# Performance work log

Hardware: AMD Instinct MI355X
Metric: run time of the kernel (lower is better)

## Reference

```python
import jax, jax.numpy as jnp
import numpy as np

M, K, N = 2048, 4096, 11008
Q_ABS_MAX = 128.0  # x_scaled_abs_max_fp for w8a8
Q_MIN, Q_MAX = -128, 127


def setup_inputs() -> dict:
    key = jax.random.key(0)
    k1, k2, k3, k4 = jax.random.split(key, 4)
    x = jax.random.normal(k1, (M, K), dtype=jnp.float32)
    # pre-quantized int8 weight, stored [K, N] (transposed layout as in quantize_weights)
    w_q = jax.random.randint(k2, (K, N), Q_MIN, Q_MAX + 1, dtype=jnp.int32).astype(jnp.int8)
    bias = jax.random.normal(k3, (N,), dtype=jnp.float32) * 0.01
    # per-tensor weight dequant scale (q_scale of the quantized weight)
    y_scale = jax.random.uniform(k4, (1,), dtype=jnp.float32, minval=0.001, maxval=0.02)
    return {"x": x, "w_q": w_q, "bias": bias, "y_scale": y_scale}


def reference(x, w_q, bias, y_scale):
    # dynamic per-tensor activation quantization: scale = max|x| / 128
    x_scale = jnp.max(jnp.abs(x)) / jnp.float32(Q_ABS_MAX)
    x_q = jnp.clip(jnp.round(x / x_scale), Q_MIN, Q_MAX).astype(jnp.int8)
    c = jnp.matmul(x_q.astype(jnp.int32), w_q.astype(jnp.int32))
    # dequantize + bias
    y = c.astype(jnp.float32) * (x_scale * y_scale[0]) + bias
    return y
```

## Files before the change

### kernel.cpp

```cpp
#include <hip/hip_runtime.h>
#include <stdint.h>

#define M_DIM 2048
#define K_DIM 4096
#define N_DIM 11008

typedef int v4i __attribute__((ext_vector_type(4)));

#define WS_XQ_OFF   65536ull
#define WS_WT_OFF   8454144ull
#define WS_FULL_BYTES (8454144ull + 45088768ull)
#define WS_SMALL_BYTES 8454144ull

static __device__ __forceinline__ void llds16(const void* g, void* l) {
  __builtin_amdgcn_global_load_lds(
      reinterpret_cast<const uint32_t __attribute__((address_space(1)))*>(
          reinterpret_cast<uintptr_t>(g)),
      reinterpret_cast<uint32_t __attribute__((address_space(3)))*>(
          reinterpret_cast<uintptr_t>(l)),
      16, 0, 0);
}

__global__ __launch_bounds__(256) void absmax_kernel(const float* __restrict__ x,
                                                     float* __restrict__ part) {
  __shared__ float red[256];
  const int g = blockIdx.x * 256 + threadIdx.x;
  const float4* x4 = reinterpret_cast<const float4*>(x);
  float m = 0.f;
#pragma unroll
  for (int i = 0; i < 8; ++i) {
    float4 v = x4[(size_t)i * 262144 + g];
    m = fmaxf(m, fmaxf(fmaxf(fabsf(v.x), fabsf(v.y)),
                       fmaxf(fabsf(v.z), fabsf(v.w))));
  }
  red[threadIdx.x] = m;
  __syncthreads();
  for (int s = 128; s > 0; s >>= 1) {
    if (threadIdx.x < s) red[threadIdx.x] = fmaxf(red[threadIdx.x], red[threadIdx.x + s]);
    __syncthreads();
  }
  if (threadIdx.x == 0) part[blockIdx.x] = red[0];
}

__global__ __launch_bounds__(256) void finalize_scale(const float* __restrict__ part,
                                                      const float* __restrict__ y_scale,
                                                      float* __restrict__ scales) {
  __shared__ float red[256];
  const int t = threadIdx.x;
  float m = fmaxf(fmaxf(part[t], part[t + 256]), fmaxf(part[t + 512], part[t + 768]));
  red[t] = m;
  __syncthreads();
  for (int s = 128; s > 0; s >>= 1) {
    if (t < s) red[t] = fmaxf(red[t], red[t + s]);
    __syncthreads();
  }
  if (t == 0) {
    float xs = red[0] * (1.0f / 128.0f);
    scales[0] = xs;
    scales[1] = xs * y_scale[0];
  }
}

__global__ __launch_bounds__(256) void quant_kernel(const float* __restrict__ x,
                                                    const float* __restrict__ scales,
                                                    signed char* __restrict__ xq) {
  const float s = scales[0];
  const size_t t = (size_t)blockIdx.x * 256 + threadIdx.x;
  const float4* x4 = reinterpret_cast<const float4*>(x) + t * 4;
  v4i o;
#pragma unroll
  for (int i = 0; i < 4; ++i) {
    float4 v = x4[i];
    int q0 = (int)rintf(v.x / s);
    int q1 = (int)rintf(v.y / s);
    int q2 = (int)rintf(v.z / s);
    int q3 = (int)rintf(v.w / s);
    q0 = max(-128, min(127, q0));
    q1 = max(-128, min(127, q1));
    q2 = max(-128, min(127, q2));
    q3 = max(-128, min(127, q3));
    o[i] = (q0 & 255) | ((q1 & 255) << 8) | ((q2 & 255) << 16) | ((q3 & 255) << 24);
  }
  *reinterpret_cast<v4i*>(xq + t * 16) = o;
}

__global__ __launch_bounds__(256) void transpose_pack(const int* __restrict__ w,
                                                      signed char* __restrict__ wt) {
  __shared__ int tile[64 * 65];
  const int t = threadIdx.x;
  const int n0 = blockIdx.x * 64;
  const int k0 = blockIdx.y * 64;
#pragma unroll
  for (int p = 0; p < 4; ++p) {
    const int id = p * 256 + t;
    const int r = id >> 4;
    const int c4 = id & 15;
    v4i v = *reinterpret_cast<const v4i*>(w + (size_t)(k0 + r) * N_DIM + n0 + c4 * 4);
    tile[r * 65 + c4 * 4 + 0] = v[0];
    tile[r * 65 + c4 * 4 + 1] = v[1];
    tile[r * 65 + c4 * 4 + 2] = v[2];
    tile[r * 65 + c4 * 4 + 3] = v[3];
  }
  __syncthreads();
  const int nl = t >> 2;
  const int kseg = t & 3;
  v4i o;
#pragma unroll
  for (int q = 0; q < 4; ++q) {
    const int kb = kseg * 16 + q * 4;
    int b0 = tile[(kb + 0) * 65 + nl] & 255;
    int b1 = tile[(kb + 1) * 65 + nl] & 255;
    int b2 = tile[(kb + 2) * 65 + nl] & 255;
    int b3 = tile[(kb + 3) * 65 + nl] & 255;
    o[q] = b0 | (b1 << 8) | (b2 << 16) | (b3 << 24);
  }
  *reinterpret_cast<v4i*>(wt + (size_t)(n0 + nl) * K_DIM + k0 + kseg * 16) = o;
}

__global__ __launch_bounds__(256) void gemm_i8(
    const signed char* __restrict__ xq, const signed char* __restrict__ wt,
    const float* __restrict__ scales, const float* __restrict__ bias,
    float* __restrict__ y) {
  __shared__ __align__(16) signed char lds_a[128 * 64];
  __shared__ __align__(16) signed char lds_b[128 * 64];
  const int tid = threadIdx.x;
  const int m0 = blockIdx.y * 128;
  const int n0 = blockIdx.x * 128;

  const int srow = tid >> 2;
  const int sseg = tid & 3;
  const int sgseg = sseg ^ ((srow ^ (srow >> 2)) & 3);
  const signed char* ga0 = xq + (size_t)(m0 + srow) * K_DIM + sgseg * 16;
  const signed char* gb0 = wt + (size_t)(n0 + srow) * K_DIM + sgseg * 16;
  signed char* la0 = lds_a + tid * 16;
  signed char* lb0 = lds_b + tid * 16;

  const int lane = tid & 63;
  const int wid = tid >> 6;
  const int wr = wid >> 1;
  const int wc = wid & 1;
  const int l15 = lane & 15;
  const int kc = lane >> 4;
  const int rslot = (kc ^ ((l15 ^ (l15 >> 2)) & 3)) * 16;
  const signed char* pa = lds_a + (wr * 64 + l15) * 64 + rslot;
  const signed char* pb = lds_b + (wc * 64 + l15) * 64 + rslot;

  v4i acc[4][4] = {};

  for (int kt = 0; kt < K_DIM / 64; ++kt) {
    const int ko = kt * 64;
    llds16(ga0 + ko, la0);
    llds16(ga0 + ko + (size_t)64 * K_DIM, la0 + 4096);
    llds16(gb0 + ko, lb0);
    llds16(gb0 + ko + (size_t)64 * K_DIM, lb0 + 4096);
    __syncthreads();
    v4i a4[4], b4[4];
#pragma unroll
    for (int m = 0; m < 4; ++m) a4[m] = *reinterpret_cast<const v4i*>(pa + m * 1024);
#pragma unroll
    for (int n = 0; n < 4; ++n) b4[n] = *reinterpret_cast<const v4i*>(pb + n * 1024);
#pragma unroll
    for (int m = 0; m < 4; ++m)
#pragma unroll
      for (int n = 0; n < 4; ++n)
        acc[m][n] = __builtin_amdgcn_mfma_i32_16x16x64_i8(a4[m], b4[n], acc[m][n], 0, 0, 0);
    __syncthreads();
  }

  const float s = scales[1];
#pragma unroll
  for (int n = 0; n < 4; ++n) {
    const int col = n0 + wc * 64 + n * 16 + l15;
    const float bv = bias[col];
#pragma unroll
    for (int m = 0; m < 4; ++m) {
      const int r0 = m0 + wr * 64 + m * 16 + kc * 4;
#pragma unroll
      for (int j = 0; j < 4; ++j)
        y[(size_t)(r0 + j) * N_DIM + col] = (float)acc[m][n][j] * s + bv;
    }
  }
}

#if defined(__has_builtin)
#if __has_builtin(__builtin_amdgcn_sdot4)
#define HAVE_SDOT4 1
#endif
#endif

static __device__ __forceinline__ int dot4(int a, int b, int c) {
#ifdef HAVE_SDOT4
  return __builtin_amdgcn_sdot4(a, b, c, false);
#else
  c += (int)(signed char)(a) * (int)(signed char)(b);
  c += (int)(signed char)(a >> 8) * (int)(signed char)(b >> 8);
  c += (int)(signed char)(a >> 16) * (int)(signed char)(b >> 16);
  c += (int)(signed char)(a >> 24) * (int)(signed char)(b >> 24);
  return c;
#endif
}

__global__ __launch_bounds__(256) void gemm_fallback(
    const signed char* __restrict__ xq, const int* __restrict__ w,
    const float* __restrict__ scales, const float* __restrict__ bias,
    float* __restrict__ y) {
  __shared__ int lds_a[64 * 17];
  __shared__ int lds_b[64 * 17];
  const int t = threadIdx.x;
  const int m0 = blockIdx.y * 64;
  const int n0 = blockIdx.x * 64;
  const int my = (t >> 4) * 4;
  const int nx = (t & 15) * 4;
  int acc[4][4] = {};
  for (int kt = 0; kt < K_DIM / 64; ++kt) {
    const int k0 = kt * 64;
    {
      const int r = t >> 2, sg = t & 3;
      v4i v = *reinterpret_cast<const v4i*>(xq + (size_t)(m0 + r) * K_DIM + k0 + sg * 16);
      lds_a[r * 17 + sg * 4 + 0] = v[0];
      lds_a[r * 17 + sg * 4 + 1] = v[1];
      lds_a[r * 17 + sg * 4 + 2] = v[2];
      lds_a[r * 17 + sg * 4 + 3] = v[3];
    }
    {
      const int n = t & 63, bkk = (t >> 6) * 4;
#pragma unroll
      for (int q = 0; q < 4; ++q) {
        const int kk = bkk + q;
        int b0 = w[(size_t)(k0 + kk * 4 + 0) * N_DIM + n0 + n] & 255;
        int b1 = w[(size_t)(k0 + kk * 4 + 1) * N_DIM + n0 + n] & 255;
        int b2 = w[(size_t)(k0 + kk * 4 + 2) * N_DIM + n0 + n] & 255;
        int b3 = w[(size_t)(k0 + kk * 4 + 3) * N_DIM + n0 + n] & 255;
        lds_b[n * 17 + kk] = b0 | (b1 << 8) | (b2 << 16) | (b3 << 24);
      }
    }
    __syncthreads();
#pragma unroll
    for (int kk = 0; kk < 16; ++kk) {
      int a[4], b[4];
#pragma unroll
      for (int i = 0; i < 4; ++i) a[i] = lds_a[(my + i) * 17 + kk];
#pragma unroll
      for (int j = 0; j < 4; ++j) b[j] = lds_b[(nx + j) * 17 + kk];
#pragma unroll
      for (int i = 0; i < 4; ++i)
#pragma unroll
        for (int j = 0; j < 4; ++j) acc[i][j] = dot4(a[i], b[j], acc[i][j]);
    }
    __syncthreads();
  }
  const float s = scales[1];
#pragma unroll
  for (int i = 0; i < 4; ++i)
#pragma unroll
    for (int j = 0; j < 4; ++j)
      y[(size_t)(m0 + my + i) * N_DIM + n0 + nx + j] =
          (float)acc[i][j] * s + bias[n0 + nx + j];
}

extern "C" void kernel_launch(void* const* d_in, const int* in_sizes, int n_in,
                              void* d_out, int out_size, void* d_ws, size_t ws_size,
                              hipStream_t stream) {
  (void)in_sizes; (void)n_in; (void)out_size;
  const float* x = (const float*)d_in[0];
  const int* w = (const int*)d_in[1];
  const float* bias = (const float*)d_in[2];
  const float* yscale = (const float*)d_in[3];
  float* y = (float*)d_out;
  char* ws = (char*)d_ws;
  float* scales = (float*)(ws);
  float* part = (float*)(ws + 1024);
  signed char* xq = (signed char*)(ws + WS_XQ_OFF);
  signed char* wt = (signed char*)(ws + WS_WT_OFF);

  if (ws_size < WS_SMALL_BYTES) return;

  absmax_kernel<<<1024, 256, 0, stream>>>(x, part);
  finalize_scale<<<1, 256, 0, stream>>>(part, yscale, scales);
  quant_kernel<<<2048, 256, 0, stream>>>(x, scales, xq);
  if (ws_size >= WS_FULL_BYTES) {
    transpose_pack<<<dim3(N_DIM / 64, K_DIM / 64), 256, 0, stream>>>(w, wt);
    gemm_i8<<<dim3(N_DIM / 128, M_DIM / 128), 256, 0, stream>>>(xq, wt, scales, bias, y);
  } else {
    gemm_fallback<<<dim3(N_DIM / 64, M_DIM / 64), 256, 0, stream>>>(xq, w, scales, bias, y);
  }
}
```

Baseline: 191.7 us.

## Triple-buffer int8 GEMM with 128x256 tiles and swizzled block order

Replaces the single-buffered 128x128 int8 MFMA GEMM with a 128x256 tile kernel that uses a three-stage LDS ring. Global-to-LDS loads for tile k+2 are issued before computing tile k, with a single barrier per iteration. A 1D grid with an XCD-aware swizzle maps blocks to tiles for better L2 reuse. The aim is to hide load latency and raise MFMA density per LDS read. In exchange, register pressure rises to 32 accumulators per wave, and LDS use grows to 72KB per block, which may limit occupancy.

```diff
diff --git a/kernel.cpp b/kernel.cpp
--- a/kernel.cpp
+++ b/kernel.cpp
@@ -117,64 +117,104 @@
   *reinterpret_cast<v4i*>(wt + (size_t)(n0 + nl) * K_DIM + k0 + kseg * 16) = o;
 }
 
-__global__ __launch_bounds__(256) void gemm_i8(
+#define TILE_B 24576
+#define NT_K   (K_DIM / 64)
+
+__global__ __launch_bounds__(256, 2) void gemm_i8_v2(
     const signed char* __restrict__ xq, const signed char* __restrict__ wt,
     const float* __restrict__ scales, const float* __restrict__ bias,
     float* __restrict__ y) {
-  __shared__ __align__(16) signed char lds_a[128 * 64];
-  __shared__ __align__(16) signed char lds_b[128 * 64];
+  __shared__ __align__(16) signed char smem[3 * TILE_B];
   const int tid = threadIdx.x;
-  const int m0 = blockIdx.y * 128;
-  const int n0 = blockIdx.x * 128;
+
+  const int bid = blockIdx.x;
+  const int swz = (bid & 7) * 86 + (bid >> 3);
+  const int m0 = (swz & 15) * 128;
+  const int n0 = (swz >> 4) * 256;
 
   const int srow = tid >> 2;
   const int sseg = tid & 3;
   const int sgseg = sseg ^ ((srow ^ (srow >> 2)) & 3);
-  const signed char* ga0 = xq + (size_t)(m0 + srow) * K_DIM + sgseg * 16;
-  const signed char* gb0 = wt + (size_t)(n0 + srow) * K_DIM + sgseg * 16;
-  signed char* la0 = lds_a + tid * 16;
-  signed char* lb0 = lds_b + tid * 16;
+  const signed char* gA = xq + (size_t)(m0 + srow) * K_DIM + sgseg * 16;
+  const signed char* gB = wt + (size_t)(n0 + srow) * K_DIM + sgseg * 16;
+  signed char* const l0 = smem + tid * 16;
+
+#define STAGE(kt, soff)                                                   \
+  do {                                                                    \
+    const size_t ko_ = (size_t)(kt) * 64;                                 \
+    llds16(gA + ko_,                       l0 + (soff));                  \
+    llds16(gA + ko_ + (size_t)64 * K_DIM,  l0 + (soff) + 4096);           \
+    llds16(gB + ko_,                       l0 + (soff) + 8192);           \
+    llds16(gB + ko_ + (size_t)64 * K_DIM,  l0 + (soff) + 12288);          \
+    llds16(gB + ko_ + (size_t)128 * K_DIM, l0 + (soff) + 16384);          \
+    llds16(gB + ko_ + (size_t)192 * K_DIM, l0 + (soff) + 20480);          \
+  } while (0)
 
   const int lane = tid & 63;
   const int wid = tid >> 6;
-  const int wr = wid >> 1;
-  const int wc = wid & 1;
+  const int wm = wid >> 1;
+  const int wn = wid & 1;
   const int l15 = lane & 15;
   const int kc = lane >> 4;
   const int rslot = (kc ^ ((l15 ^ (l15 >> 2)) & 3)) * 16;
-  const signed char* pa = lds_a + (wr * 64 + l15) * 64 + rslot;
-  const signed char* pb = lds_b + (wc * 64 + l15) * 64 + rslot;
-
-  v4i acc[4][4] = {};
-
-  for (int kt = 0; kt < K_DIM / 64; ++kt) {
-    const int ko = kt * 64;
-    llds16(ga0 + ko, la0);
-    llds16(ga0 + ko + (size_t)64 * K_DIM, la0 + 4096);
-    llds16(gb0 + ko, lb0);
-    llds16(gb0 + ko + (size_t)64 * K_DIM, lb0 + 4096);
-    __syncthreads();
-    v4i a4[4], b4[4];
-#pragma unroll
-    for (int m = 0; m < 4; ++m) a4[m] = *reinterpret_cast<const v4i*>(pa + m * 1024);
-#pragma unroll
-    for (int n = 0; n < 4; ++n) b4[n] = *reinterpret_cast<const v4i*>(pb + n * 1024);
-#pragma unroll
-    for (int m = 0; m < 4; ++m)
-#pragma unroll
-      for (int n = 0; n < 4; ++n)
-        acc[m][n] = __builtin_amdgcn_mfma_i32_16x16x64_i8(a4[m], b4[n], acc[m][n], 0, 0, 0);
-    __syncthreads();
-  }
+  const int cA = (wm * 64 + l15) * 64 + rslot;
+  const int cB = 8192 + (wn * 128 + l15) * 64 + rslot;
+
+  v4i acc[4][8] = {};
+
+#define COMPUTE(roff)                                                        \
+  do {                                                                       \
+    const signed char* bp_ = smem + (roff);                                  \
+    v4i a_[4], b_[8];                                                        \
+    _Pragma("unroll")                                                        \
+    for (int m_ = 0; m_ < 4; ++m_)                                           \
+      a_[m_] = *reinterpret_cast<const v4i*>(bp_ + cA + m_ * 1024);          \
+    _Pragma("unroll")                                                        \
+    for (int n_ = 0; n_ < 8; ++n_)                                           \
+      b_[n_] = *reinterpret_cast<const v4i*>(bp_ + cB + n_ * 1024);          \
+    _Pragma("unroll")                                                        \
+    for (int m_ = 0; m_ < 4; ++m_)                                           \
+      _Pragma("unroll")                                                      \
+      for (int n_ = 0; n_ < 8; ++n_)                                         \
+        acc[m_][n_] = __builtin_amdgcn_mfma_i32_16x16x64_i8(                 \
+            a_[m_], b_[n_], acc[m_][n_], 0, 0, 0);                           \
+  } while (0)
+
+  STAGE(0, 0);
+  STAGE(1, TILE_B);
+
+  int rOff = 0;
+  int sOff = 2 * TILE_B;
+  for (int t = 0; t < NT_K - 2; ++t) {
+    asm volatile("s_waitcnt vmcnt(6)" ::: "memory");
+    __builtin_amdgcn_s_barrier();
+    __builtin_amdgcn_sched_barrier(0);
+    STAGE(t + 2, sOff);
+    COMPUTE(rOff);
+    rOff = (rOff == 2 * TILE_B) ? 0 : rOff + TILE_B;
+    sOff = (sOff == 2 * TILE_B) ? 0 : sOff + TILE_B;
+  }
+  asm volatile("s_waitcnt vmcnt(6)" ::: "memory");
+  __builtin_amdgcn_s_barrier();
+  __builtin_amdgcn_sched_barrier(0);
+  COMPUTE(rOff);
+  rOff = (rOff == 2 * TILE_B) ? 0 : rOff + TILE_B;
+  asm volatile("s_waitcnt vmcnt(0)" ::: "memory");
+  __builtin_amdgcn_s_barrier();
+  __builtin_amdgcn_sched_barrier(0);
+  COMPUTE(rOff);
+
+#undef STAGE
+#undef COMPUTE
 
   const float s = scales[1];
 #pragma unroll
-  for (int n = 0; n < 4; ++n) {
-    const int col = n0 + wc * 64 + n * 16 + l15;
+  for (int n = 0; n < 8; ++n) {
+    const int col = n0 + wn * 128 + n * 16 + l15;
     const float bv = bias[col];
 #pragma unroll
     for (int m = 0; m < 4; ++m) {
-      const int r0 = m0 + wr * 64 + m * 16 + kc * 4;
+      const int r0 = m0 + wm * 64 + m * 16 + kc * 4;
 #pragma unroll
       for (int j = 0; j < 4; ++j)
         y[(size_t)(r0 + j) * N_DIM + col] = (float)acc[m][n][j] * s + bv;
@@ -280,7 +320,7 @@
   quant_kernel<<<2048, 256, 0, stream>>>(x, scales, xq);
   if (ws_size >= WS_FULL_BYTES) {
     transpose_pack<<<dim3(N_DIM / 64, K_DIM / 64), 256, 0, stream>>>(w, wt);
-    gemm_i8<<<dim3(N_DIM / 128, M_DIM / 128), 256, 0, stream>>>(xq, wt, scales, bias, y);
+    gemm_i8_v2<<<(M_DIM / 128) * (N_DIM / 256), 256, 0, stream>>>(xq, wt, scales, bias, y);
   } else {
     gemm_fallback<<<dim3(N_DIM / 64, M_DIM / 64), 256, 0, stream>>>(xq, w, scales, bias, y);
   }
```

Result: faster. 172.4 us (-10.1%).
